# Kernel tuning notes

Measured on AMD Instinct MI355X. Metric: run time of the kernel, lower is better.

The kernel has to match this reference:

```python
import jax, jax.numpy as jnp
import numpy as np

H = 32                         # LSTM_size
K = 3                          # k_value
NK, ND, NU = 4 * K + 2, K, K   # kernel / down / up step counts
T = NK + ND + NU
NEG = -1e9                     # finite mask value (avoids -inf NaNs)


def setup_inputs() -> dict:
    key = jax.random.key(0)
    ks = jax.random.split(key, 12)
    u = lambda k, s: jax.random.uniform(k, s, jnp.float32, -0.1, 0.1)
    return {
        "w_ih": u(ks[0], (4 * H, H)),
        "w_hh": u(ks[1], (4 * H, H)),
        "b_ih": u(ks[2], (4 * H,)),
        "b_hh": u(ks[3], (4 * H,)),
        "g_emb": u(ks[4], (1, H)),
        "emb_kernel": u(ks[5], (8, H)),
        "emb_down": u(ks[6], (3, H)),
        "emb_up": u(ks[7], (3, H)),
        "w_kernel": u(ks[8], (8, H)),
        "w_down": u(ks[9], (3, H)),
        "w_up": u(ks[10], (3, H)),
        "uniform_noise": jax.random.uniform(ks[11], (T, 8), jnp.float32),
    }


def _pad8(w):
    # zero-pad a [n<=8, H] table/head to [8, H]
    return jnp.pad(w, ((0, 8 - w.shape[0]), (0, 0)))


def _forward(w_ih, w_hh, b_ih, b_hh, g_emb, emb_kernel, emb_down, emb_up,
             w_kernel, w_down, w_up, uniform_noise):
    # Per-step projection heads [T, 8, H]; 3-class heads zero-padded to 8 and masked.
    proj = jnp.concatenate([
        jnp.broadcast_to(w_kernel, (NK, 8, H)),
        jnp.broadcast_to(_pad8(w_down), (ND, 8, H)),
        jnp.broadcast_to(_pad8(w_up), (NU, 8, H)),
    ])
    # Per-step embedding table used to embed the sampled action for the NEXT step.
    emb = jnp.concatenate([
        jnp.broadcast_to(emb_kernel, (NK, 8, H)),
        jnp.broadcast_to(_pad8(emb_down), (ND, 8, H)),
        jnp.broadcast_to(_pad8(emb_up), (NU, 8, H)),
    ])
    m3 = jnp.array([1, 1, 1, 0, 0, 0, 0, 0], dtype=bool)
    mask = jnp.concatenate([
        jnp.ones((NK, 8), dtype=bool),
        jnp.broadcast_to(m3, (ND, 8)),
        jnp.broadcast_to(m3, (NU, 8)),
    ])
    # Gumbel-max categorical sampling noise.
    gumbel = -jnp.log(-jnp.log(uniform_noise * (1.0 - 1e-6) + 1e-7))

    def step(carry, xs):
        h, c, x = carry                                   # h, c, x: [H]
        Wp, Et, msk, g = xs
        # Torch LSTM cell: gates = W_ih x + b_ih + W_hh h + b_hh, order i,f,g,o
        gates = w_ih @ x + b_ih + w_hh @ h + b_hh         # [4H]
        i, f, gg, o = jnp.split(gates, 4)
        c = jax.nn.sigmoid(f) * c + jax.nn.sigmoid(i) * jnp.tanh(gg)
        h = jax.nn.sigmoid(o) * jnp.tanh(c)
        logits = jnp.where(msk, Wp @ h, NEG)              # [8]
        logp = jax.nn.log_softmax(logits)
        s = jnp.argmax(logits + g)                        # Categorical sample
        p = jnp.where(msk, jnp.exp(logp), 0.0)
        ent = -jnp.sum(p * jnp.where(msk, logp, 0.0))
        return (h, c, Et[s]), (logp[s], ent, s)

    init = (jnp.zeros((H,), jnp.float32), jnp.zeros((H,), jnp.float32), g_emb[0])
    _, (lps, ents, samples) = jax.lax.scan(step, init, (proj, emb, mask, gumbel))
    # stats = [sample_log_prob, sample_entropy]
    return jnp.stack([jnp.sum(lps), jnp.sum(ents)]), samples


def reference(w_ih, w_hh, b_ih, b_hh, g_emb, emb_kernel, emb_down, emb_up,
              w_kernel, w_down, w_up, uniform_noise):
    return _forward(w_ih, w_hh, b_ih, b_hh, g_emb, emb_kernel, emb_down, emb_up,
                    w_kernel, w_down, w_up, uniform_noise)
```

## Files before the change

### kernel.cpp

```cpp
#include <hip/hip_runtime.h>

#define HH 32
#define TT 20

__device__ __forceinline__ float sigmoidf_(float x) {
    return 1.0f / (1.0f + expf(-x));
}

__global__ __launch_bounds__(64, 1) void controller_kernel(
    const float* __restrict__ w_ih,
    const float* __restrict__ w_hh,
    const float* __restrict__ b_ih,
    const float* __restrict__ b_hh,
    const float* __restrict__ g_emb,
    const float* __restrict__ emb_kernel,
    const float* __restrict__ emb_down,
    const float* __restrict__ emb_up,
    const float* __restrict__ w_kernel,
    const float* __restrict__ w_down,
    const float* __restrict__ w_up,
    const float* __restrict__ noise,
    float* __restrict__ out)
{
    const int t = threadIdx.x;

    __shared__ __align__(16) float xh_s[64];
    __shared__ float head_t[32 * 16];
    __shared__ float emb_s[14 * 32];
    __shared__ float gum_s[TT * 8];

    float w0[64], w1[64];
    {
        const float4* i0 = (const float4*)(w_ih + t * HH);
        const float4* h0 = (const float4*)(w_hh + t * HH);
        const float4* i1 = (const float4*)(w_ih + (t + 64) * HH);
        const float4* h1 = (const float4*)(w_hh + (t + 64) * HH);
#pragma unroll
        for (int q = 0; q < 8; ++q) {
            float4 a = i0[q]; w0[q*4+0]=a.x; w0[q*4+1]=a.y; w0[q*4+2]=a.z; w0[q*4+3]=a.w;
            float4 b = h0[q]; w0[32+q*4+0]=b.x; w0[32+q*4+1]=b.y; w0[32+q*4+2]=b.z; w0[32+q*4+3]=b.w;
            float4 c = i1[q]; w1[q*4+0]=c.x; w1[q*4+1]=c.y; w1[q*4+2]=c.z; w1[q*4+3]=c.w;
            float4 d = h1[q]; w1[32+q*4+0]=d.x; w1[32+q*4+1]=d.y; w1[32+q*4+2]=d.z; w1[32+q*4+3]=d.w;
        }
    }
    const float bias0 = b_ih[t] + b_hh[t];
    const float bias1 = b_ih[t + 64] + b_hh[t + 64];

    for (int idx = t; idx < 14 * 32; idx += 64) {
        const int r = idx >> 5, j = idx & 31;
        float hv, ev;
        if (r < 8)       { hv = w_kernel[r * 32 + j];        ev = emb_kernel[r * 32 + j]; }
        else if (r < 11) { hv = w_down[(r - 8) * 32 + j];    ev = emb_down[(r - 8) * 32 + j]; }
        else             { hv = w_up[(r - 11) * 32 + j];     ev = emb_up[(r - 11) * 32 + j]; }
        head_t[j * 16 + r] = hv;
        emb_s[idx] = ev;
    }
    for (int idx = t; idx < TT * 8; idx += 64) {
        const float u = noise[idx];
        gum_s[idx] = -logf(-logf(u * (1.0f - 1e-6f) + 1e-7f));
    }
    if (t < HH) xh_s[t] = g_emb[t];
    else        xh_s[t] = 0.0f;
    float c_reg = 0.0f;
    __syncthreads();

    float lp_sum = 0.0f, ent_sum = 0.0f;

    const float4* xh4 = (const float4*)xh_s;

    for (int step = 0; step < TT; ++step) {
        float a0 = bias0, a0b = 0.0f, a1 = bias1, a1b = 0.0f;
#pragma unroll
        for (int q = 0; q < 16; ++q) {
            const float4 u = xh4[q];
            const int j = q * 4;
            if (q & 1) {
                a0b += w0[j+0]*u.x; a0b += w0[j+1]*u.y; a0b += w0[j+2]*u.z; a0b += w0[j+3]*u.w;
                a1b += w1[j+0]*u.x; a1b += w1[j+1]*u.y; a1b += w1[j+2]*u.z; a1b += w1[j+3]*u.w;
            } else {
                a0 += w0[j+0]*u.x; a0 += w0[j+1]*u.y; a0 += w0[j+2]*u.z; a0 += w0[j+3]*u.w;
                a1 += w1[j+0]*u.x; a1 += w1[j+1]*u.y; a1 += w1[j+2]*u.z; a1 += w1[j+3]*u.w;
            }
        }
        a0 += a0b; a1 += a1b;

        const float fo0 = __shfl(a0, (t & 31) + 32);
        const float fo1 = __shfl(a1, (t & 31) + 32);

        if (t < HH) {
            const float ig = sigmoidf_(a0);
            const float fg = sigmoidf_(fo0);
            const float gg = tanhf(a1);
            const float og = sigmoidf_(fo1);
            c_reg = fg * c_reg + ig * gg;
            xh_s[HH + t] = og * tanhf(c_reg);
        }
        __syncthreads();

        const int n     = (step < 14) ? 8 : 3;
        const int rbase = (step < 14) ? 0 : ((step < 17) ? 8 : 11);

        float l = -1e9f;
        if (t < 8 && t < n) {
            float s0 = 0.0f, s1 = 0.0f;
#pragma unroll
            for (int j = 0; j < HH; j += 2) {
                s0 += head_t[j * 16 + rbase + t]       * xh_s[HH + j];
                s1 += head_t[(j + 1) * 16 + rbase + t] * xh_s[HH + j + 1];
            }
            l = s0 + s1;
        }

        float m = l;
#pragma unroll
        for (int msk = 1; msk <= 4; msk <<= 1) m = fmaxf(m, __shfl_xor(m, msk));

        const float e  = expf(l - m);
        float S = e, T = e * l;
#pragma unroll
        for (int msk = 1; msk <= 4; msk <<= 1) {
            S += __shfl_xor(S, msk);
            T += __shfl_xor(T, msk);
        }

        const float g = (t < 8) ? gum_s[step * 8 + t] : 0.0f;
        float v = l + g; int idx = t & 7; float lr = l;
#pragma unroll
        for (int msk = 1; msk <= 4; msk <<= 1) {
            const float ov  = __shfl_xor(v, msk);
            const int   oi  = __shfl_xor(idx, msk);
            const float olr = __shfl_xor(lr, msk);
            const bool take = (ov > v) || (ov == v && oi < idx);
            v = take ? ov : v; idx = take ? oi : idx; lr = take ? olr : lr;
        }

        if (t == 0) {
            const float lse = m + logf(S);
            lp_sum  += lr - lse;
            ent_sum += lse - T / S;
            out[2 + step] = (float)idx;
        }
        const int s = __shfl(idx, 0);

        if (t < HH) xh_s[t] = emb_s[(rbase + s) * 32 + t];
        __syncthreads();
    }

    if (t == 0) {
        out[0] = lp_sum;
        out[1] = ent_sum;
    }
}

extern "C" void kernel_launch(void* const* d_in, const int* in_sizes, int n_in,
                              void* d_out, int out_size, void* d_ws, size_t ws_size,
                              hipStream_t stream) {
    (void)in_sizes; (void)n_in; (void)out_size; (void)d_ws; (void)ws_size;
    const float* w_ih       = (const float*)d_in[0];
    const float* w_hh       = (const float*)d_in[1];
    const float* b_ih       = (const float*)d_in[2];
    const float* b_hh       = (const float*)d_in[3];
    const float* g_emb      = (const float*)d_in[4];
    const float* emb_kernel = (const float*)d_in[5];
    const float* emb_down   = (const float*)d_in[6];
    const float* emb_up     = (const float*)d_in[7];
    const float* w_kernel   = (const float*)d_in[8];
    const float* w_down     = (const float*)d_in[9];
    const float* w_up       = (const float*)d_in[10];
    const float* noise      = (const float*)d_in[11];
    float* out = (float*)d_out;

    hipLaunchKernelGGL(controller_kernel, dim3(1), dim3(64), 0, stream,
                       w_ih, w_hh, b_ih, b_hh, g_emb, emb_kernel, emb_down,
                       emb_up, w_kernel, w_down, w_up, noise, out);
}
```

Baseline: 107.3 us.

## Parallelize head projection across wave, use packed FMA and fast intrinsics

Head logits are now computed by all 64 lanes, each doing a 4-element partial dot product followed by an xor-shuffle reduction, instead of 8 lanes doing serial 32-long loops. The gate matvec uses 2-wide vector float multiplies so the compiler can emit packed FMAs. Sigmoid, tanh, exp and log go through the hardware exp2, rcp and log intrinsics. Softmax now skips the max subtraction and folds the sum reductions into the argmax shuffle loop, which shortens the serial dependency chain per step. Dropping the max subtraction is safe only because the logits are small, and the fast intrinsics give up some precision.

```diff
diff --git a/kernel.cpp b/kernel.cpp
--- a/kernel.cpp
+++ b/kernel.cpp
@@ -3,8 +3,16 @@
 #define HH 32
 #define TT 20
 
-__device__ __forceinline__ float sigmoidf_(float x) {
-    return 1.0f / (1.0f + expf(-x));
+typedef float v2f __attribute__((ext_vector_type(2)));
+
+#define LOG2E  1.4426950408889634f
+#define LN2    0.6931471805599453f
+
+__device__ __forceinline__ float fsig(float x) {
+    return __builtin_amdgcn_rcpf(1.0f + __builtin_amdgcn_exp2f(-x * LOG2E));
+}
+__device__ __forceinline__ float ftanh(float x) {
+    return 1.0f - 2.0f * __builtin_amdgcn_rcpf(1.0f + __builtin_amdgcn_exp2f(x * (2.0f * LOG2E)));
 }
 
 __global__ __launch_bounds__(64, 1) void controller_kernel(
@@ -25,11 +33,11 @@
     const int t = threadIdx.x;
 
     __shared__ __align__(16) float xh_s[64];
-    __shared__ float head_t[32 * 16];
+    __shared__ __align__(16) float head_pre[3 * 64 * 4];
     __shared__ float emb_s[14 * 32];
     __shared__ float gum_s[TT * 8];
 
-    float w0[64], w1[64];
+    v2f w0[32], w1[32];
     {
         const float4* i0 = (const float4*)(w_ih + t * HH);
         const float4* h0 = (const float4*)(w_hh + t * HH);
@@ -37,23 +45,34 @@
         const float4* h1 = (const float4*)(w_hh + (t + 64) * HH);
 #pragma unroll
         for (int q = 0; q < 8; ++q) {
-            float4 a = i0[q]; w0[q*4+0]=a.x; w0[q*4+1]=a.y; w0[q*4+2]=a.z; w0[q*4+3]=a.w;
-            float4 b = h0[q]; w0[32+q*4+0]=b.x; w0[32+q*4+1]=b.y; w0[32+q*4+2]=b.z; w0[32+q*4+3]=b.w;
-            float4 c = i1[q]; w1[q*4+0]=c.x; w1[q*4+1]=c.y; w1[q*4+2]=c.z; w1[q*4+3]=c.w;
-            float4 d = h1[q]; w1[32+q*4+0]=d.x; w1[32+q*4+1]=d.y; w1[32+q*4+2]=d.z; w1[32+q*4+3]=d.w;
+            float4 a = i0[q]; w0[2*q] = (v2f){a.x, a.y};      w0[2*q+1] = (v2f){a.z, a.w};
+            float4 b = h0[q]; w0[16+2*q] = (v2f){b.x, b.y};   w0[16+2*q+1] = (v2f){b.z, b.w};
+            float4 c = i1[q]; w1[2*q] = (v2f){c.x, c.y};      w1[2*q+1] = (v2f){c.z, c.w};
+            float4 d = h1[q]; w1[16+2*q] = (v2f){d.x, d.y};   w1[16+2*q+1] = (v2f){d.z, d.w};
         }
     }
     const float bias0 = b_ih[t] + b_hh[t];
     const float bias1 = b_ih[t + 64] + b_hh[t + 64];
 
+#pragma unroll
+    for (int bi = 0; bi < 3; ++bi) {
+        const int rb  = (bi == 0) ? 0 : ((bi == 1) ? 8 : 11);
+        const int row = rb + (t & 7);
+        const int ch  = (t >> 3) * 4;
+        float4 v = make_float4(0.f, 0.f, 0.f, 0.f);
+        if (row < 14) {
+            const float* W = (row < 8)  ? (w_kernel + row * 32)
+                           : (row < 11) ? (w_down + (row - 8) * 32)
+                                        : (w_up + (row - 11) * 32);
+            v = *(const float4*)(W + ch);
+        }
+        *(float4*)(head_pre + (bi * 64 + t) * 4) = v;
+    }
     for (int idx = t; idx < 14 * 32; idx += 64) {
         const int r = idx >> 5, j = idx & 31;
-        float hv, ev;
-        if (r < 8)       { hv = w_kernel[r * 32 + j];        ev = emb_kernel[r * 32 + j]; }
-        else if (r < 11) { hv = w_down[(r - 8) * 32 + j];    ev = emb_down[(r - 8) * 32 + j]; }
-        else             { hv = w_up[(r - 11) * 32 + j];     ev = emb_up[(r - 11) * 32 + j]; }
-        head_t[j * 16 + r] = hv;
-        emb_s[idx] = ev;
+        emb_s[idx] = (r < 8)  ? emb_kernel[r * 32 + j]
+                   : (r < 11) ? emb_down[(r - 8) * 32 + j]
+                              : emb_up[(r - 11) * 32 + j];
     }
     for (int idx = t; idx < TT * 8; idx += 64) {
         const float u = noise[idx];
@@ -69,80 +88,65 @@
     const float4* xh4 = (const float4*)xh_s;
 
     for (int step = 0; step < TT; ++step) {
-        float a0 = bias0, a0b = 0.0f, a1 = bias1, a1b = 0.0f;
+        v2f s0a = {0.f, 0.f}, s0b = {0.f, 0.f}, s1a = {0.f, 0.f}, s1b = {0.f, 0.f};
 #pragma unroll
         for (int q = 0; q < 16; ++q) {
-            const float4 u = xh4[q];
-            const int j = q * 4;
-            if (q & 1) {
-                a0b += w0[j+0]*u.x; a0b += w0[j+1]*u.y; a0b += w0[j+2]*u.z; a0b += w0[j+3]*u.w;
-                a1b += w1[j+0]*u.x; a1b += w1[j+1]*u.y; a1b += w1[j+2]*u.z; a1b += w1[j+3]*u.w;
-            } else {
-                a0 += w0[j+0]*u.x; a0 += w0[j+1]*u.y; a0 += w0[j+2]*u.z; a0 += w0[j+3]*u.w;
-                a1 += w1[j+0]*u.x; a1 += w1[j+1]*u.y; a1 += w1[j+2]*u.z; a1 += w1[j+3]*u.w;
-            }
+            const float4 xv = xh4[q];
+            const v2f u0 = {xv.x, xv.y};
+            const v2f u1 = {xv.z, xv.w};
+            s0a += w0[2*q] * u0;  s0b += w0[2*q+1] * u1;
+            s1a += w1[2*q] * u0;  s1b += w1[2*q+1] * u1;
         }
-        a0 += a0b; a1 += a1b;
+        const float a0 = bias0 + ((s0a.x + s0a.y) + (s0b.x + s0b.y));
+        const float a1 = bias1 + ((s1a.x + s1a.y) + (s1b.x + s1b.y));
 
-        const float fo0 = __shfl(a0, (t & 31) + 32);
-        const float fo1 = __shfl(a1, (t & 31) + 32);
+        const float fo0 = __shfl_xor(a0, 32);
+        const float fo1 = __shfl_xor(a1, 32);
 
         if (t < HH) {
-            const float ig = sigmoidf_(a0);
-            const float fg = sigmoidf_(fo0);
-            const float gg = tanhf(a1);
-            const float og = sigmoidf_(fo1);
+            const float ig = fsig(a0);
+            const float fg = fsig(fo0);
+            const float gg = ftanh(a1);
+            const float og = fsig(fo1);
             c_reg = fg * c_reg + ig * gg;
-            xh_s[HH + t] = og * tanhf(c_reg);
+            xh_s[HH + t] = og * ftanh(c_reg);
         }
         __syncthreads();
 
         const int n     = (step < 14) ? 8 : 3;
+        const int bi    = (step < 14) ? 0 : ((step < 17) ? 1 : 2);
         const int rbase = (step < 14) ? 0 : ((step < 17) ? 8 : 11);
 
-        float l = -1e9f;
-        if (t < 8 && t < n) {
-            float s0 = 0.0f, s1 = 0.0f;
+        const float4 hp = *(const float4*)(head_pre + (bi * 64 + t) * 4);
+        const float4 hv = *(const float4*)(xh_s + HH + (t >> 3) * 4);
+        float p = hp.x * hv.x + hp.y * hv.y + hp.z * hv.z + hp.w * hv.w;
+        p += __shfl_xor(p, 8);
+        p += __shfl_xor(p, 16);
+        p += __shfl_xor(p, 32);
+        const float l = ((t & 7) < n) ? p : -1e9f;
+
+        float e = __builtin_amdgcn_exp2f(l * LOG2E);
+        float S = e, T = e * l;
+        float v = l + gum_s[step * 8 + (t & 7)];
+        int   idx = t & 7;
+        float lr  = l;
 #pragma unroll
-            for (int j = 0; j < HH; j += 2) {
-                s0 += head_t[j * 16 + rbase + t]       * xh_s[HH + j];
-                s1 += head_t[(j + 1) * 16 + rbase + t] * xh_s[HH + j + 1];
-            }
-            l = s0 + s1;
-        }
-
-        float m = l;
-#pragma unroll
-        for (int msk = 1; msk <= 4; msk <<= 1) m = fmaxf(m, __shfl_xor(m, msk));
-
-        const float e  = expf(l - m);
-        float S = e, T = e * l;
-#pragma unroll
-        for (int msk = 1; msk <= 4; msk <<= 1) {
-            S += __shfl_xor(S, msk);
-            T += __shfl_xor(T, msk);
-        }
-
-        const float g = (t < 8) ? gum_s[step * 8 + t] : 0.0f;
-        float v = l + g; int idx = t & 7; float lr = l;
-#pragma unroll
-        for (int msk = 1; msk <= 4; msk <<= 1) {
-            const float ov  = __shfl_xor(v, msk);
-            const int   oi  = __shfl_xor(idx, msk);
-            const float olr = __shfl_xor(lr, msk);
+        for (int m = 1; m <= 4; m <<= 1) {
+            S += __shfl_xor(S, m);
+            T += __shfl_xor(T, m);
+            const float ov  = __shfl_xor(v, m);
+            const int   oi  = __shfl_xor(idx, m);
+            const float olr = __shfl_xor(lr, m);
             const bool take = (ov > v) || (ov == v && oi < idx);
             v = take ? ov : v; idx = take ? oi : idx; lr = take ? olr : lr;
         }
 
-        if (t == 0) {
-            const float lse = m + logf(S);
-            lp_sum  += lr - lse;
-            ent_sum += lse - T / S;
-            out[2 + step] = (float)idx;
-        }
-        const int s = __shfl(idx, 0);
+        const float lse = __builtin_amdgcn_logf(S) * LN2;
+        lp_sum  += lr - lse;
+        ent_sum += lse - T * __builtin_amdgcn_rcpf(S);
+        if (t == 0) out[2 + step] = (float)idx;
 
-        if (t < HH) xh_s[t] = emb_s[(rbase + s) * 32 + t];
+        if (t < HH) xh_s[t] = emb_s[(rbase + idx) * 32 + t];
         __syncthreads();
     }
 
```

New measurement: 95.60 us. -10.9%, faster.
